# Kernel optimization log

Measured on AMD Instinct MI355X. Metric: run time of the kernel, lower is better.

The kernel has to match this reference:

```python
import math
import jax, jax.numpy as jnp
import numpy as np

TWO_PI = 2.0 * math.pi
BETA = 1.0
K_COUP = 1.0
A_ANC = 0.08
OMEGA_ANC = TWO_PI * 200.0
B, P, N = 64, 256, 4096


def setup_inputs() -> dict:
    key = jax.random.key(0)
    k1, k2, k3 = jax.random.split(key, 3)
    t = jax.random.uniform(k1, (1,), dtype=jnp.float32)
    phi = jax.random.uniform(k2, (B, N), dtype=jnp.float32) * TWO_PI
    xi = jax.random.uniform(k3, (P, N), dtype=jnp.float32) * TWO_PI
    return {"t": t, "phi": phi, "xi": xi}


def reference(t, phi, xi):
    # diff: (B, P, N)
    diff = phi[:, None, :] - xi[None, :, :]
    m = jnp.cos(diff).sum(-1)                      # (B, P)
    weights = jax.nn.softmax(BETA * m / N, axis=-1)  # (B, P)
    coupling = jnp.einsum('bp,bpn->bn', weights, jnp.sin(diff))  # (B, N)
    dphi = K_COUP * coupling + A_ANC * jnp.sin(OMEGA_ANC * t - phi)
    return dphi
```

## Files before the change

### kernel.cpp

```cpp
#include <hip/hip_runtime.h>
#include <hip/hip_fp16.h>
#include <math.h>
#include <stdint.h>

#define B_SZ 64
#define P_SZ 256
#define N_SZ 4096
#define NCA 32
#define A_ANC 0.08f
#define OMEGA_ANC 1256.6370614359172f

typedef _Float16 half8 __attribute__((ext_vector_type(8)));
typedef float floatx4 __attribute__((ext_vector_type(4)));

__global__ __launch_bounds__(256) void k_xp(const float* __restrict__ xi,
                                            __half2* __restrict__ XP) {
    int idx = blockIdx.x * 256 + threadIdx.x;
    float s, c;
    __sincosf(xi[idx], &s, &c);
    XP[idx] = __floats2half2_rn(c, s);
}

__global__ __launch_bounds__(256) void k_mpart_mfma(const float* __restrict__ phi,
                                                    const __half2* __restrict__ XP,
                                                    float* __restrict__ m_part) {
    const int bt = blockIdx.x & 3;
    const int pt = blockIdx.x >> 2;
    const int w  = threadIdx.x >> 6;
    const int lane = threadIdx.x & 63;
    const int m = lane & 15;
    const int q = lane >> 4;

    const int c  = blockIdx.y * 4 + w;
    const int n0 = c * 128;
    const int b_row = bt * 16 + m;
    const int p_row = pt * 16 + m;

    floatx4 acc = {0.f, 0.f, 0.f, 0.f};
#pragma unroll
    for (int s = 0; s < 8; ++s) {
        const int nb = n0 + s * 16 + q * 4;
        float4 ph = *(const float4*)&phi[b_row * N_SZ + nb];
        half8 bf = *(const half8*)&XP[p_row * N_SZ + nb];
        half8 af;
        float ss, cc;
        __sincosf(ph.x, &ss, &cc); af[0] = (_Float16)cc; af[1] = (_Float16)ss;
        __sincosf(ph.y, &ss, &cc); af[2] = (_Float16)cc; af[3] = (_Float16)ss;
        __sincosf(ph.z, &ss, &cc); af[4] = (_Float16)cc; af[5] = (_Float16)ss;
        __sincosf(ph.w, &ss, &cc); af[6] = (_Float16)cc; af[7] = (_Float16)ss;
        acc = __builtin_amdgcn_mfma_f32_16x16x32_f16(af, bf, acc, 0, 0, 0);
    }
#pragma unroll
    for (int r = 0; r < 4; ++r) {
        int b = bt * 16 + q * 4 + r;
        m_part[(c * 64 + b) * 256 + pt * 16 + m] = acc[r];
    }
}

__global__ __launch_bounds__(256) void k_weights(const float* __restrict__ m_part,
                                                 _Float16* __restrict__ Wh) {
    const int b = blockIdx.x;
    const int tid = threadIdx.x;
    const int wv = tid >> 6;
    __shared__ float sred[8];

    float msum = 0.f;
#pragma unroll 8
    for (int c = 0; c < NCA; ++c)
        msum += m_part[(c * 64 + b) * 256 + tid];
    float logit = msum * (1.0f / 4096.0f);

    float v = logit;
    for (int o = 32; o > 0; o >>= 1) v = fmaxf(v, __shfl_xor(v, o));
    if ((tid & 63) == 0) sred[wv] = v;
    __syncthreads();
    float mx = fmaxf(fmaxf(sred[0], sred[1]), fmaxf(sred[2], sred[3]));
    float e = __expf(logit - mx);
    v = e;
    for (int o = 32; o > 0; o >>= 1) v += __shfl_xor(v, o);
    if ((tid & 63) == 0) sred[4 + wv] = v;
    __syncthreads();
    float s = sred[4] + sred[5] + sred[6] + sred[7];
    Wh[b * 256 + tid] = (_Float16)(e / s);
}

__global__ __launch_bounds__(256) void k_coupling_mfma(const __half2* __restrict__ XP,
                                                       const _Float16* __restrict__ Wh,
                                                       const float* __restrict__ phi,
                                                       const float* __restrict__ t_ptr,
                                                       float* __restrict__ out) {
    const int mt = blockIdx.x;
    const int ct = blockIdx.y * 4 + (threadIdx.x >> 6);
    const int lane = threadIdx.x & 63;
    const int cl = lane & 15;
    const int q  = lane >> 4;

    const int col  = ct * 16 + cl;
    const int n    = col >> 1;
    const int comp = col & 1;

    const _Float16* wrow = Wh + (mt * 16 + cl) * 256;
    const uint32_t* xp32 = (const uint32_t*)XP;

    floatx4 acc = {0.f, 0.f, 0.f, 0.f};
#pragma unroll
    for (int s = 0; s < 8; ++s) {
        const int k0 = s * 32 + q * 8;
        half8 af = *(const half8*)&wrow[k0];
        half8 bf;
#pragma unroll
        for (int j = 0; j < 8; ++j) {
            uint32_t v = xp32[(k0 + j) * N_SZ + n];
            uint16_t h = (uint16_t)(comp ? (v >> 16) : (v & 0xffffu));
            bf[j] = __builtin_bit_cast(_Float16, h);
        }
        acc = __builtin_amdgcn_mfma_f32_16x16x32_f16(af, bf, acc, 0, 0, 0);
    }

    float aS0 = __shfl_xor(acc[0], 1);
    float aS1 = __shfl_xor(acc[1], 1);
    float aS2 = __shfl_xor(acc[2], 1);
    float aS3 = __shfl_xor(acc[3], 1);
    if (!comp) {
        const float wt = OMEGA_ANC * t_ptr[0];
        float aC[4] = {acc[0], acc[1], acc[2], acc[3]};
        float aS[4] = {aS0, aS1, aS2, aS3};
#pragma unroll
        for (int r = 0; r < 4; ++r) {
            int b = mt * 16 + q * 4 + r;
            float ph = phi[b * N_SZ + n];
            float ss, cc;
            __sincosf(ph, &ss, &cc);
            out[b * N_SZ + n] =
                fmaf(A_ANC, __sinf(wt - ph), ss * aC[r] - cc * aS[r]);
        }
    }
}

extern "C" void kernel_launch(void* const* d_in, const int* in_sizes, int n_in,
                              void* d_out, int out_size, void* d_ws, size_t ws_size,
                              hipStream_t stream) {
    const float* t   = (const float*)d_in[0];
    const float* phi = (const float*)d_in[1];
    const float* xi  = (const float*)d_in[2];
    float* out = (float*)d_out;

    char* w = (char*)d_ws;
    __half2* XP     = (__half2*)w;
    float* m_part   = (float*)(w + 4u * 1024 * 1024);
    _Float16* Wh    = (_Float16*)(w + 6u * 1024 * 1024);

    k_xp<<<(P_SZ * N_SZ) / 256, 256, 0, stream>>>(xi, XP);
    k_mpart_mfma<<<dim3(64, 8), 256, 0, stream>>>(phi, XP, m_part);
    k_weights<<<64, 256, 0, stream>>>(m_part, Wh);
    k_coupling_mfma<<<dim3(4, 128), 256, 0, stream>>>(XP, Wh, phi, t, out);
}
```

Before: 78.53 us.

## Fuse xi sincos into m-partial kernel and store transposed table for coupling

Drops the separate k_xp launch. The m-partial MFMA kernel now computes cos/sin of xi itself, and blocks with bt==0 write the packed half2 table transposed, as [n][p]. The coupling kernel then reads contiguous 16-byte vectors along p and extracts the needed half with byte-permute, replacing eight strided 4-byte gathers per step. The cost is that every b-tile recomputes the xi sincos (4x redundant), and the transposed writes are scattered uint32 stores.

Measured after the change: 76.25 us. -2.9%, faster.

```diff
diff --git a/kernel.cpp b/kernel.cpp
--- a/kernel.cpp
+++ b/kernel.cpp
@@ -13,16 +13,22 @@
 typedef _Float16 half8 __attribute__((ext_vector_type(8)));
 typedef float floatx4 __attribute__((ext_vector_type(4)));
 
-__global__ __launch_bounds__(256) void k_xp(const float* __restrict__ xi,
-                                            __half2* __restrict__ XP) {
-    int idx = blockIdx.x * 256 + threadIdx.x;
-    float s, c;
-    __sincosf(xi[idx], &s, &c);
-    XP[idx] = __floats2half2_rn(c, s);
+__device__ __forceinline__ uint32_t permsel(uint32_t hi, uint32_t lo, uint32_t sel) {
+#if __has_builtin(__builtin_amdgcn_perm)
+    return __builtin_amdgcn_perm(hi, lo, sel);
+#else
+    unsigned long long v = ((unsigned long long)hi << 32) | lo;
+    uint32_t r = 0;
+#pragma unroll
+    for (int i = 0; i < 4; ++i)
+        r |= (uint32_t)((v >> (8 * ((sel >> (8 * i)) & 7))) & 0xff) << (8 * i);
+    return r;
+#endif
 }
 
 __global__ __launch_bounds__(256) void k_mpart_mfma(const float* __restrict__ phi,
-                                                    const __half2* __restrict__ XP,
+                                                    const float* __restrict__ xi,
+                                                    uint32_t* __restrict__ XPT,
                                                     float* __restrict__ m_part) {
     const int bt = blockIdx.x & 3;
     const int pt = blockIdx.x >> 2;
@@ -41,13 +47,24 @@
     for (int s = 0; s < 8; ++s) {
         const int nb = n0 + s * 16 + q * 4;
         float4 ph = *(const float4*)&phi[b_row * N_SZ + nb];
-        half8 bf = *(const half8*)&XP[p_row * N_SZ + nb];
-        half8 af;
+        float4 xv = *(const float4*)&xi[p_row * N_SZ + nb];
+        half8 af, bf;
         float ss, cc;
         __sincosf(ph.x, &ss, &cc); af[0] = (_Float16)cc; af[1] = (_Float16)ss;
         __sincosf(ph.y, &ss, &cc); af[2] = (_Float16)cc; af[3] = (_Float16)ss;
         __sincosf(ph.z, &ss, &cc); af[4] = (_Float16)cc; af[5] = (_Float16)ss;
         __sincosf(ph.w, &ss, &cc); af[6] = (_Float16)cc; af[7] = (_Float16)ss;
+        __sincosf(xv.x, &ss, &cc); bf[0] = (_Float16)cc; bf[1] = (_Float16)ss;
+        __sincosf(xv.y, &ss, &cc); bf[2] = (_Float16)cc; bf[3] = (_Float16)ss;
+        __sincosf(xv.z, &ss, &cc); bf[4] = (_Float16)cc; bf[5] = (_Float16)ss;
+        __sincosf(xv.w, &ss, &cc); bf[6] = (_Float16)cc; bf[7] = (_Float16)ss;
+        if (bt == 0) {
+            uint4 bi = __builtin_bit_cast(uint4, bf);
+            XPT[(nb + 0) * P_SZ + p_row] = bi.x;
+            XPT[(nb + 1) * P_SZ + p_row] = bi.y;
+            XPT[(nb + 2) * P_SZ + p_row] = bi.z;
+            XPT[(nb + 3) * P_SZ + p_row] = bi.w;
+        }
         acc = __builtin_amdgcn_mfma_f32_16x16x32_f16(af, bf, acc, 0, 0, 0);
     }
 #pragma unroll
@@ -84,7 +101,7 @@
     Wh[b * 256 + tid] = (_Float16)(e / s);
 }
 
-__global__ __launch_bounds__(256) void k_coupling_mfma(const __half2* __restrict__ XP,
+__global__ __launch_bounds__(256) void k_coupling_mfma(const uint32_t* __restrict__ XPT,
                                                        const _Float16* __restrict__ Wh,
                                                        const float* __restrict__ phi,
                                                        const float* __restrict__ t_ptr,
@@ -98,22 +115,24 @@
     const int col  = ct * 16 + cl;
     const int n    = col >> 1;
     const int comp = col & 1;
+    const uint32_t sel = comp ? 0x07060302u : 0x05040100u;
 
     const _Float16* wrow = Wh + (mt * 16 + cl) * 256;
-    const uint32_t* xp32 = (const uint32_t*)XP;
+    const uint32_t* xrow = XPT + n * P_SZ;
 
     floatx4 acc = {0.f, 0.f, 0.f, 0.f};
 #pragma unroll
     for (int s = 0; s < 8; ++s) {
         const int k0 = s * 32 + q * 8;
         half8 af = *(const half8*)&wrow[k0];
-        half8 bf;
-#pragma unroll
-        for (int j = 0; j < 8; ++j) {
-            uint32_t v = xp32[(k0 + j) * N_SZ + n];
-            uint16_t h = (uint16_t)(comp ? (v >> 16) : (v & 0xffffu));
-            bf[j] = __builtin_bit_cast(_Float16, h);
-        }
+        uint4 v0 = *(const uint4*)&xrow[k0];
+        uint4 v1 = *(const uint4*)&xrow[k0 + 4];
+        uint4 bi;
+        bi.x = permsel(v0.y, v0.x, sel);
+        bi.y = permsel(v0.w, v0.z, sel);
+        bi.z = permsel(v1.y, v1.x, sel);
+        bi.w = permsel(v1.w, v1.z, sel);
+        half8 bf = __builtin_bit_cast(half8, bi);
         acc = __builtin_amdgcn_mfma_f32_16x16x32_f16(af, bf, acc, 0, 0, 0);
     }
 
@@ -146,12 +165,11 @@
     float* out = (float*)d_out;
 
     char* w = (char*)d_ws;
-    __half2* XP     = (__half2*)w;
+    uint32_t* XPT   = (uint32_t*)w;
     float* m_part   = (float*)(w + 4u * 1024 * 1024);
     _Float16* Wh    = (_Float16*)(w + 6u * 1024 * 1024);
 
-    k_xp<<<(P_SZ * N_SZ) / 256, 256, 0, stream>>>(xi, XP);
-    k_mpart_mfma<<<dim3(64, 8), 256, 0, stream>>>(phi, XP, m_part);
+    k_mpart_mfma<<<dim3(64, 8), 256, 0, stream>>>(phi, xi, XPT, m_part);
     k_weights<<<64, 256, 0, stream>>>(m_part, Wh);
-    k_coupling_mfma<<<dim3(4, 128), 256, 0, stream>>>(XP, Wh, phi, t, out);
+    k_coupling_mfma<<<dim3(4, 128), 256, 0, stream>>>(XPT, Wh, phi, t, out);
 }
```
